# Kernel tuning notes

Measured on AMD Instinct MI355X. Metric: run time of the kernel, lower is better.

## Reference

```python
import jax, jax.numpy as jnp
import numpy as np
from jax import lax

STRIDE = 16
ANCHOR_BASE = 16
PRE_NMS = 6000
POST_NMS = 2000
NMS_THRESH = 0.7


def _generate_anchors(base_size=16, ratios=(0.5, 1.0, 2.0), scales=(8, 16, 32)):
    w = h = float(base_size)
    x_ctr = 0.5 * (w - 1)
    y_ctr = 0.5 * (h - 1)
    size = w * h
    anchors = []
    for r in ratios:
        ws = np.round(np.sqrt(size / r))
        hs = np.round(ws * r)
        for s in scales:
            wss, hss = ws * s, hs * s
            anchors.append([x_ctr - 0.5 * (wss - 1), y_ctr - 0.5 * (hss - 1),
                            x_ctr + 0.5 * (wss - 1), y_ctr + 0.5 * (hss - 1)])
    return np.array(anchors, dtype=np.float32)  # [9,4]


def _all_anchors(width, height, stride):
    base = _generate_anchors(ANCHOR_BASE)  # [A,4]
    sx = np.arange(width, dtype=np.float32) * stride
    gy, gx = np.meshgrid(np.arange(height, dtype=np.float32) * stride, sx, indexing='ij')
    shifts = np.stack([gx.ravel(), gy.ravel(), gx.ravel(), gy.ravel()], axis=1)  # [K,4] h-major
    return jnp.asarray((shifts[:, None, :] + base[None, :, :]).reshape(-1, 4))  # [K*A,4]


def setup_inputs() -> dict:
    key = jax.random.key(0)
    k1, k2 = jax.random.split(key)
    H = W = 64
    bbox_deltas = jax.random.normal(k1, (1, 36, H, W), dtype=jnp.float32)
    scores = jax.random.uniform(k2, (1, 2, 9 * H, W), dtype=jnp.float32)
    return {"bbox_deltas": bbox_deltas, "scores": scores, "im_w": 1024, "im_h": 1024}


def reference(bbox_deltas, scores, im_w, im_h):
    H, W = bbox_deltas.shape[2], bbox_deltas.shape[3]
    # fg scores: reshape [1,2,9H,W] -> [1,18,H,W], take channels 9:18
    sc = scores.reshape(1, 18, H, W)[:, 9:, :, :].transpose(0, 2, 3, 1).reshape(-1)
    dl = bbox_deltas.transpose(0, 2, 3, 1).reshape(-1, 4)
    anchors = _all_anchors(W, H, STRIDE)

    # bbox_transform_inv (decode)
    aw = anchors[:, 2] - anchors[:, 0] + 1.0
    ah = anchors[:, 3] - anchors[:, 1] + 1.0
    acx = anchors[:, 0] + 0.5 * aw
    acy = anchors[:, 1] + 0.5 * ah
    pcx = dl[:, 0] * aw + acx
    pcy = dl[:, 1] * ah + acy
    pw = jnp.exp(dl[:, 2]) * aw
    ph = jnp.exp(dl[:, 3]) * ah
    x1 = jnp.clip(pcx - 0.5 * pw, 0.0, im_w - 1.0)
    y1 = jnp.clip(pcy - 0.5 * ph, 0.0, im_h - 1.0)
    x2 = jnp.clip(pcx + 0.5 * pw, 0.0, im_w - 1.0)
    y2 = jnp.clip(pcy + 0.5 * ph, 0.0, im_h - 1.0)
    props = jnp.stack([x1, y1, x2, y2], axis=1)

    # min-size filter
    thresh = 16.0 * (float(im_h) / float(im_w))
    keep_f = ((x2 - x1 + 1.0) >= thresh) & ((y2 - y1 + 1.0) >= thresh)
    sc_m = jnp.where(keep_f, sc, -jnp.inf)

    # pre-NMS top-k by score
    top_sc, idx = lax.top_k(sc_m, PRE_NMS)
    top_p = props[idx]  # [PRE_NMS,4], sorted by score desc
    valid = jnp.isfinite(top_sc)

    # pairwise IoU (with +1 box convention, as in py_cpu_nms)
    bx1, by1, bx2, by2 = top_p[:, 0], top_p[:, 1], top_p[:, 2], top_p[:, 3]
    areas = (bx2 - bx1 + 1.0) * (by2 - by1 + 1.0)
    iw = jnp.maximum(jnp.minimum(bx2[:, None], bx2[None, :]) - jnp.maximum(bx1[:, None], bx1[None, :]) + 1.0, 0.0)
    ih = jnp.maximum(jnp.minimum(by2[:, None], by2[None, :]) - jnp.maximum(by1[:, None], by1[None, :]) + 1.0, 0.0)
    inter = iw * ih
    iou = inter / (areas[:, None] + areas[None, :] - inter)
    sup = iou > NMS_THRESH  # [N,N]

    ar = jnp.arange(PRE_NMS)

    def body(i, keep):
        row = sup[i] & keep[i] & (ar > i)
        return keep & (~row)

    keep = lax.fori_loop(0, PRE_NMS, body, valid)

    # take first POST_NMS kept (in score order), scatter into fixed-size output
    rank = jnp.cumsum(keep.astype(jnp.int32)) - 1
    sel = keep & (rank < POST_NMS)
    dst = jnp.where(sel, rank, POST_NMS)  # invalid rows dumped into slot POST_NMS
    out_b = jnp.zeros((POST_NMS + 1, 4), dtype=jnp.float32).at[dst].set(
        jnp.where(sel[:, None], top_p, 0.0))[:POST_NMS]
    out_s = jnp.zeros((POST_NMS + 1,), dtype=jnp.float32).at[dst].set(
        jnp.where(sel, top_sc, 0.0))[:POST_NMS]
    blob = jnp.concatenate([jnp.zeros((POST_NMS, 1), dtype=jnp.float32), out_b], axis=1)
    return blob, out_s[:, None]
```

## Files before the change

kernel.cpp:

```cpp
#include <hip/hip_runtime.h>
#include <math.h>

typedef unsigned int u32;
typedef unsigned long long u64;

#define NANCH   36864
#define PRE     6000
#define POST    2000
#define NWORDS  94

#define OFF_PROPS   ((size_t)0)
#define OFF_SV      ((size_t)589824)
#define OFF_TOPBOX  ((size_t)884736)
#define OFF_SORTED  ((size_t)980992)
#define OFF_SEL     ((size_t)1029120)
#define OFF_TOPKEY  ((size_t)1077248)
#define OFF_INVALW  ((size_t)1101312)
#define OFF_MASK    ((size_t)1102080)
#define OFF_ZERO    ((size_t)5614080)
#define OFF_H1      (OFF_ZERO)
#define OFF_H2      (OFF_H1 + 262144)
#define OFF_H3      (OFF_H2 + 262144)
#define OFF_CTRL    (OFF_H3 + 262144)
#define OFF_KEEPW   (OFF_CTRL + 256)
#define OFF_RANK    (OFF_KEEPW + 768)
#define ZERO_BYTES  ((size_t)(262144*3 + 256 + 768 + 24064))

__device__ __constant__ float BA[9][4] = {
  {-84.f,-40.f,99.f,55.f},   {-176.f,-88.f,191.f,103.f}, {-360.f,-184.f,375.f,199.f},
  {-56.f,-56.f,71.f,71.f},   {-120.f,-120.f,135.f,135.f},{-248.f,-248.f,263.f,263.f},
  {-36.f,-80.f,51.f,95.f},   {-80.f,-168.f,95.f,183.f},  {-168.f,-344.f,183.f,359.f}};

__global__ void decode_k(const float* __restrict__ deltas, const float* __restrict__ scores,
                         const int* __restrict__ imw_p, const int* __restrict__ imh_p,
                         float4* __restrict__ props, u64* __restrict__ sortvals) {
  #pragma clang fp contract(off)
  int i = blockIdx.x * 256 + threadIdx.x;
  if (i >= NANCH) return;
  int a = i % 9;
  int pix = i / 9;
  int x = pix & 63, y = pix >> 6;

  float sc = scores[(9 + a) * 4096 + pix];
  float d0 = deltas[(a * 4 + 0) * 4096 + pix];
  float d1 = deltas[(a * 4 + 1) * 4096 + pix];
  float d2 = deltas[(a * 4 + 2) * 4096 + pix];
  float d3 = deltas[(a * 4 + 3) * 4096 + pix];

  float gx = (float)(x * 16), gy = (float)(y * 16);
  float ax1 = gx + BA[a][0], ay1 = gy + BA[a][1];
  float ax2 = gx + BA[a][2], ay2 = gy + BA[a][3];
  float aw = ax2 - ax1 + 1.0f, ah = ay2 - ay1 + 1.0f;
  float acx = ax1 + 0.5f * aw, acy = ay1 + 0.5f * ah;

  float pcx = d0 * aw + acx;
  float pcy = d1 * ah + acy;
  float pw = (float)exp((double)d2) * aw;
  float ph = (float)exp((double)d3) * ah;

  float imw1 = (float)imw_p[0] - 1.0f, imh1 = (float)imh_p[0] - 1.0f;
  float x1 = fminf(fmaxf(pcx - 0.5f * pw, 0.0f), imw1);
  float y1 = fminf(fmaxf(pcy - 0.5f * ph, 0.0f), imh1);
  float x2 = fminf(fmaxf(pcx + 0.5f * pw, 0.0f), imw1);
  float y2 = fminf(fmaxf(pcy + 0.5f * ph, 0.0f), imh1);
  props[i] = make_float4(x1, y1, x2, y2);

  float thresh = 16.0f * ((float)imh_p[0] / (float)imw_p[0]);
  bool keep = (x2 - x1 + 1.0f >= thresh) && (y2 - y1 + 1.0f >= thresh);
  u32 key = keep ? (__float_as_uint(sc) | 0x80000000u) : 0u;
  sortvals[i] = ((u64)key << 32) | (u64)(0xFFFFFFFFu - (u32)i);
}

__global__ void hist_k(const u64* __restrict__ sv, u32* __restrict__ hist,
                       const u32* __restrict__ ctrl, int level) {
  int i = blockIdx.x * 256 + threadIdx.x;
  if (i >= NANCH) return;
  u64 v = sv[i];
  if (level == 1) {
    atomicAdd(&hist[(u32)(v >> 48)], 1u);
  } else if (level == 2) {
    if ((u32)(v >> 48) == ctrl[0]) atomicAdd(&hist[(u32)(v >> 32) & 0xFFFFu], 1u);
  } else {
    u32 pfx = (ctrl[0] << 16) | ctrl[2];
    if ((u32)(v >> 32) == pfx) atomicAdd(&hist[(u32)v & 0xFFFFu], 1u);
  }
}

__global__ void scan_k(const u32* __restrict__ hist, u32* __restrict__ ctrl, int level) {
  __shared__ u32 part[1024];
  int t = threadIdx.x;
  u32 ssum = 0;
  for (int b = 0; b < 64; ++b) ssum += hist[t * 64 + b];
  part[t] = ssum;
  __syncthreads();
  if (t == 0) {
    u32 Rin = (level == 1) ? (u32)PRE : ctrl[(level - 1) * 2 - 1];
    u32 acc = 0; int pt;
    for (pt = 1023; pt >= 0; --pt) {
      if (acc + part[pt] >= Rin) break;
      acc += part[pt];
    }
    int chosen = pt * 64; u32 Rout = Rin;
    for (int b = pt * 64 + 63; b >= pt * 64; --b) {
      u32 h = hist[b];
      if (acc + h >= Rin) { chosen = b; Rout = Rin - acc; break; }
      acc += h;
    }
    ctrl[(level - 1) * 2] = (u32)chosen;
    ctrl[(level - 1) * 2 + 1] = Rout;
    if (level == 3) {
      u64 T = ((u64)ctrl[0] << 48) | ((u64)ctrl[2] << 32) | 0xFFFF0000ULL | (u64)(u32)chosen;
      *(u64*)(&ctrl[8]) = T;
    }
  }
}

__global__ void compact_k(const u64* __restrict__ sv, u32* __restrict__ ctrl,
                          u64* __restrict__ sel) {
  int i = blockIdx.x * 256 + threadIdx.x;
  if (i >= NANCH) return;
  u64 T = *(const u64*)(&ctrl[8]);
  u64 v = sv[i];
  if (v >= T) {
    u32 p = atomicAdd(&ctrl[6], 1u);
    sel[p] = v;
  }
}

#define JCHUNK 1500
__global__ void rank_k(const u64* __restrict__ sel, u32* __restrict__ rank) {
  __shared__ u64 sj[256];
  int i = blockIdx.x * 256 + threadIdx.x;
  u64 vi = (i < PRE) ? sel[i] : 0ULL;
  int j0 = blockIdx.y * JCHUNK;
  int j1 = min(j0 + JCHUNK, PRE);
  u32 cnt = 0;
  for (int jb = j0; jb < j1; jb += 256) {
    int nj = min(256, j1 - jb);
    __syncthreads();
    if (threadIdx.x < nj) sj[threadIdx.x] = sel[jb + threadIdx.x];
    __syncthreads();
    #pragma unroll 8
    for (int j = 0; j < nj; ++j) cnt += (u32)(sj[j] > vi);
  }
  if (i < PRE && cnt) atomicAdd(&rank[i], cnt);
}

__global__ void rankscatter_k(const u64* __restrict__ sel, const u32* __restrict__ rank,
                              u64* __restrict__ sorted) {
  int i = blockIdx.x * 256 + threadIdx.x;
  if (i < PRE) sorted[rank[i]] = sel[i];
}

__global__ void gather_k(const u64* __restrict__ sorted, const float4* __restrict__ props,
                         float4* __restrict__ topbox, u32* __restrict__ topkey,
                         u64* __restrict__ invalw) {
  int r = blockIdx.x * 64 + threadIdx.x;
  u32 key = 0;
  if (r < PRE) {
    u64 v = sorted[r];
    key = (u32)(v >> 32);
    u32 idx = 0xFFFFu - ((u32)v & 0xFFFFu);
    topbox[r] = props[idx];
    topkey[r] = key;
  }
  u64 inval = __ballot(key == 0u);
  if (threadIdx.x == 0) invalw[blockIdx.x] = inval;
}

__global__ void mask_k(const float4* __restrict__ topbox, u64* __restrict__ mask) {
  #pragma clang fp contract(off)
  __shared__ float4 cb[64];
  int jb = blockIdx.x;
  if (jb < (int)blockIdx.y) return;
  int i = blockIdx.y * 64 + threadIdx.x;
  int jj = jb * 64 + threadIdx.x;
  cb[threadIdx.x] = (jj < PRE) ? topbox[jj] : make_float4(0.f, 0.f, 0.f, 0.f);
  __syncthreads();
  if (i >= PRE) return;
  float4 b = topbox[i];
  float ai = (b.z - b.x + 1.0f) * (b.w - b.y + 1.0f);
  u64 bits = 0ULL;
  int jmax = min(64, PRE - jb * 64);
  for (int j = 0; j < jmax; ++j) {
    float4 c = cb[j];
    float aj = (c.z - c.x + 1.0f) * (c.w - c.y + 1.0f);
    float iw = fmaxf(fminf(b.z, c.z) - fmaxf(b.x, c.x) + 1.0f, 0.0f);
    float ih = fmaxf(fminf(b.w, c.w) - fmaxf(b.y, c.y) + 1.0f, 0.0f);
    float inter = iw * ih;
    float iou = inter / (ai + aj - inter);
    bits |= ((u64)(iou > 0.7f)) << j;
  }
  mask[(size_t)i * NWORDS + jb] = bits;
}

__device__ __forceinline__ u64 rl64(u64 v, int lane) {
  u32 lo = (u32)__builtin_amdgcn_readlane((int)(u32)v, lane);
  u32 hi = (u32)__builtin_amdgcn_readlane((int)(u32)(v >> 32), lane);
  return ((u64)hi << 32) | (u64)lo;
}
__device__ __forceinline__ u64 rfl64(u64 v) {
  u32 lo = (u32)__builtin_amdgcn_readfirstlane((int)(u32)v);
  u32 hi = (u32)__builtin_amdgcn_readfirstlane((int)(u32)(v >> 32));
  return ((u64)hi << 32) | (u64)lo;
}

__global__ void __launch_bounds__(1024) nms_scan_k(const u64* __restrict__ mask,
                                                   const u64* __restrict__ invalw,
                                                   u64* __restrict__ keepw) {
  __shared__ u64 Lrem[NWORDS];
  __shared__ u64 Ldiag[64];
  __shared__ u64 Lkeep;
  __shared__ int Lstop;
  const int t = threadIdx.x;
  const int g = t >> 7;
  const int w = t & 127;
  const bool loader = (w < NWORDS);
  if (t < NWORDS) Lrem[t] = invalw[t];
  if (t == 0) Lstop = 0;
  u64 rv = 0;
  u64 B0[8], B1[8], B2[8];
  int kept = 0;

#define ISSUE(bb, BUF) \
  if ((bb) < NWORDS && loader) { \
    const int row0_ = (bb) * 64 + g * 8; \
    const u64* pp_ = mask + (size_t)row0_ * NWORDS + w; \
    _Pragma("unroll") \
    for (int j = 0; j < 8; ++j) { \
      bool ok_ = (w >= (bb)) && (row0_ + j < PRE); \
      BUF[j] = ok_ ? pp_[(size_t)j * NWORDS] : 0ULL; \
    } \
  }

#define STEP(bb, BUF, BUF2) { \
    if (w == (bb)) {                      \
      atomicOr((u32*)&Lrem[(bb)], (u32)rv); \
      atomicOr(((u32*)&Lrem[(bb)]) + 1, (u32)(rv >> 32)); \
      _Pragma("unroll") \
      for (int j = 0; j < 8; ++j) Ldiag[g * 8 + j] = BUF[j]; \
    } \
    __syncthreads();                      \
    ISSUE((bb) + 2, BUF2)                 \
    if (t < 64) { \
      u64 dgl = Ldiag[t]; \
      u64 avail = ~rfl64(Lrem[(bb)]);     \
      u64 kb = 0; \
      while (avail) { \
        int i_ = __builtin_ctzll(avail); \
        kb |= 1ULL << i_; \
        u64 di_ = rl64(dgl, i_); \
        avail &= ~di_ & ~((2ULL << i_) - 1ULL);  \
      } \
      if (t == 0) { \
        keepw[(bb)] = kb; \
        Lkeep = kb; \
        kept += (int)__popcll(kb); \
        if (kept >= POST) Lstop = 1; \
      } \
    } \
    __syncthreads();                      \
    { \
      u64 kb_ = Lkeep; \
      const int base_ = g * 8; \
      _Pragma("unroll") \
      for (int j = 0; j < 8; ++j) { \
        u64 k_ = (kb_ >> (base_ + j)) & 1ULL; \
        rv |= (0ULL - k_) & BUF[j]; \
      } \
    } \
    if (Lstop) break; }

  ISSUE(0, B0)
  ISSUE(1, B1)
  for (int bb = 0; bb < NWORDS; bb += 3) {
    STEP(bb, B0, B2)
    if (bb + 1 < NWORDS) STEP(bb + 1, B1, B0)
    if (bb + 2 < NWORDS) STEP(bb + 2, B2, B1)
  }
#undef ISSUE
#undef STEP
}

__global__ void scatter_k(const u64* __restrict__ keepw, const float4* __restrict__ topbox,
                          const u32* __restrict__ topkey, float* __restrict__ out) {
  __shared__ u64 wl[NWORDS];
  __shared__ u32 pre[NWORDS];
  int t = threadIdx.x;
  if (t < NWORDS) wl[t] = keepw[t];
  __syncthreads();
  if (t == 0) {
    u32 run = 0;
    for (int w = 0; w < NWORDS; ++w) { pre[w] = run; run += (u32)__popcll(wl[w]); }
  }
  __syncthreads();
  for (int i = t; i < PRE; i += 1024) {
    int w = i >> 6;
    u64 word = wl[w];
    if ((word >> (i & 63)) & 1ULL) {
      u32 rank = pre[w] + (u32)__popcll(word & ((1ULL << (i & 63)) - 1ULL));
      if (rank < POST) {
        float4 b = topbox[i];
        out[rank * 5 + 1] = b.x;
        out[rank * 5 + 2] = b.y;
        out[rank * 5 + 3] = b.z;
        out[rank * 5 + 4] = b.w;
        out[10000 + rank] = __uint_as_float(topkey[i] & 0x7FFFFFFFu);
      }
    }
  }
}

extern "C" void kernel_launch(void* const* d_in, const int* in_sizes, int n_in,
                              void* d_out, int out_size, void* d_ws, size_t ws_size,
                              hipStream_t stream) {
  const float* deltas = (const float*)d_in[0];
  const float* scores = (const float*)d_in[1];
  const int* imw = (const int*)d_in[2];
  const int* imh = (const int*)d_in[3];
  char* ws = (char*)d_ws;

  float4* props   = (float4*)(ws + OFF_PROPS);
  u64*    svals   = (u64*)(ws + OFF_SV);
  float4* topbox  = (float4*)(ws + OFF_TOPBOX);
  u64*    sorted  = (u64*)(ws + OFF_SORTED);
  u64*    sel     = (u64*)(ws + OFF_SEL);
  u32*    topkey  = (u32*)(ws + OFF_TOPKEY);
  u64*    invalw  = (u64*)(ws + OFF_INVALW);
  u64*    maskb   = (u64*)(ws + OFF_MASK);
  u32*    h1      = (u32*)(ws + OFF_H1);
  u32*    h2      = (u32*)(ws + OFF_H2);
  u32*    h3      = (u32*)(ws + OFF_H3);
  u32*    ctrl    = (u32*)(ws + OFF_CTRL);
  u64*    keepw   = (u64*)(ws + OFF_KEEPW);
  u32*    rankb   = (u32*)(ws + OFF_RANK);

  hipMemsetAsync(ws + OFF_ZERO, 0, ZERO_BYTES, stream);
  hipMemsetAsync(d_out, 0, 12000 * sizeof(float), stream);

  decode_k<<<144, 256, 0, stream>>>(deltas, scores, imw, imh, props, svals);

  hist_k<<<144, 256, 0, stream>>>(svals, h1, ctrl, 1);
  scan_k<<<1, 1024, 0, stream>>>(h1, ctrl, 1);
  hist_k<<<144, 256, 0, stream>>>(svals, h2, ctrl, 2);
  scan_k<<<1, 1024, 0, stream>>>(h2, ctrl, 2);
  hist_k<<<144, 256, 0, stream>>>(svals, h3, ctrl, 3);
  scan_k<<<1, 1024, 0, stream>>>(h3, ctrl, 3);

  compact_k<<<144, 256, 0, stream>>>(svals, ctrl, sel);

  dim3 rgrid(24, 4);
  rank_k<<<rgrid, 256, 0, stream>>>(sel, rankb);
  rankscatter_k<<<24, 256, 0, stream>>>(sel, rankb, sorted);

  gather_k<<<94, 64, 0, stream>>>(sorted, props, topbox, topkey, invalw);

  dim3 mgrid(NWORDS, NWORDS);
  mask_k<<<mgrid, 64, 0, stream>>>(topbox, maskb);

  nms_scan_k<<<1, 1024, 0, stream>>>(maskb, invalw, keepw);
  scatter_k<<<1, 1024, 0, stream>>>(keepw, topbox, topkey, (float*)d_out);
}
```

Measured before the change: 408.8 us.

## Fuse level-1 histogram into decode, parallelize radix scan, deepen NMS prefetch

The level-1 histogram atomic moves into the decode kernel, which removes one launch and one pass over the sort values. The threshold-finding scan replaces its serial single-thread search with wavefront shuffle reductions and a ballot. The NMS scan kernel swaps __syncthreads for a raw s_waitcnt lgkmcnt(0) plus s_barrier, and prefetches mask rows three steps ahead with four buffers instead of three. The custom barrier does not wait on global memory counters, which is safe only because the barrier-protected shared state lives in LDS. The extra buffer raises register pressure.

After: 456.3 us. +11.6%, slower.

```diff
diff --git a/kernel.cpp b/kernel.cpp
--- a/kernel.cpp
+++ b/kernel.cpp
@@ -33,7 +33,8 @@
 
 __global__ void decode_k(const float* __restrict__ deltas, const float* __restrict__ scores,
                          const int* __restrict__ imw_p, const int* __restrict__ imh_p,
-                         float4* __restrict__ props, u64* __restrict__ sortvals) {
+                         float4* __restrict__ props, u64* __restrict__ sortvals,
+                         u32* __restrict__ h1) {
   #pragma clang fp contract(off)
   int i = blockIdx.x * 256 + threadIdx.x;
   if (i >= NANCH) return;
@@ -69,6 +70,7 @@
   bool keep = (x2 - x1 + 1.0f >= thresh) && (y2 - y1 + 1.0f >= thresh);
   u32 key = keep ? (__float_as_uint(sc) | 0x80000000u) : 0u;
   sortvals[i] = ((u64)key << 32) | (u64)(0xFFFFFFFFu - (u32)i);
+  atomicAdd(&h1[key >> 16], 1u);
 }
 
 __global__ void hist_k(const u64* __restrict__ sv, u32* __restrict__ hist,
@@ -76,9 +78,7 @@
   int i = blockIdx.x * 256 + threadIdx.x;
   if (i >= NANCH) return;
   u64 v = sv[i];
-  if (level == 1) {
-    atomicAdd(&hist[(u32)(v >> 48)], 1u);
-  } else if (level == 2) {
+  if (level == 2) {
     if ((u32)(v >> 48) == ctrl[0]) atomicAdd(&hist[(u32)(v >> 32) & 0xFFFFu], 1u);
   } else {
     u32 pfx = (ctrl[0] << 16) | ctrl[2];
@@ -86,31 +86,65 @@
   }
 }
 
-__global__ void scan_k(const u32* __restrict__ hist, u32* __restrict__ ctrl, int level) {
+__global__ void __launch_bounds__(1024) scan_k(const u32* __restrict__ hist,
+                                               u32* __restrict__ ctrl, int level) {
   __shared__ u32 part[1024];
-  int t = threadIdx.x;
-  u32 ssum = 0;
-  for (int b = 0; b < 64; ++b) ssum += hist[t * 64 + b];
-  part[t] = ssum;
-  __syncthreads();
-  if (t == 0) {
-    u32 Rin = (level == 1) ? (u32)PRE : ctrl[(level - 1) * 2 - 1];
-    u32 acc = 0; int pt;
-    for (pt = 1023; pt >= 0; --pt) {
-      if (acc + part[pt] >= Rin) break;
-      acc += part[pt];
+  __shared__ u32 wtot[16], wsfx[16];
+  __shared__ int cgrp;
+  __shared__ u32 ghi;
+  const int t = threadIdx.x, w = t >> 6, l = t & 63;
+
+  for (int k = 0; k < 64; ++k) {
+    int gg = w + (k << 4);
+    u32 v = hist[gg * 64 + l];
+    for (int off = 32; off; off >>= 1) v += __shfl_down(v, off);
+    if (l == 0) part[gg] = v;
+  }
+  __syncthreads();
+
+  u32 v = part[t];
+  for (int off = 1; off < 64; off <<= 1) {
+    u32 o = __shfl_down(v, off);
+    if (l + off < 64) v += o;
+  }
+  if (l == 0) wtot[w] = v;
+  __syncthreads();
+  if (w == 0 && l < 16) {
+    u32 x = wtot[l];
+    for (int off = 1; off < 16; off <<= 1) {
+      u32 o = __shfl_down(x, off);
+      if (l + off < 16) x += o;
     }
-    int chosen = pt * 64; u32 Rout = Rin;
-    for (int b = pt * 64 + 63; b >= pt * 64; --b) {
-      u32 h = hist[b];
-      if (acc + h >= Rin) { chosen = b; Rout = Rin - acc; break; }
-      acc += h;
+    wsfx[l] = x;
+  }
+  __syncthreads();
+
+  u32 Rin = (level == 1) ? (u32)PRE : ctrl[(level - 1) * 2 - 1];
+  u32 G = v + ((w < 15) ? wsfx[w + 1] : 0);
+  u32 p = part[t];
+  if (G >= Rin && G - p < Rin) { cgrp = t; ghi = G - p; }
+  __syncthreads();
+
+  if (w == 0) {
+    int gg = cgrp;
+    u32 h = hist[gg * 64 + l];
+    u32 s = h;
+    for (int off = 1; off < 64; off <<= 1) {
+      u32 o = __shfl_down(s, off);
+      if (l + off < 64) s += o;
     }
-    ctrl[(level - 1) * 2] = (u32)chosen;
-    ctrl[(level - 1) * 2 + 1] = Rout;
-    if (level == 3) {
-      u64 T = ((u64)ctrl[0] << 48) | ((u64)ctrl[2] << 32) | 0xFFFF0000ULL | (u64)(u32)chosen;
-      *(u64*)(&ctrl[8]) = T;
+    u32 S = s + ghi;
+    u64 m = __ballot(S >= Rin);
+    int cb = 63 - __builtin_clzll(m);
+    if (l == cb) {
+      u32 Rout = Rin - (S - h);
+      int chosen = gg * 64 + cb;
+      ctrl[(level - 1) * 2] = (u32)chosen;
+      ctrl[(level - 1) * 2 + 1] = Rout;
+      if (level == 3) {
+        u64 T = ((u64)ctrl[0] << 48) | ((u64)ctrl[2] << 32) | 0xFFFF0000ULL | (u64)(u32)chosen;
+        *(u64*)(&ctrl[8]) = T;
+      }
     }
   }
 }
@@ -194,6 +228,9 @@
   mask[(size_t)i * NWORDS + jb] = bits;
 }
 
+__device__ __forceinline__ void wg_barrier() {
+  __asm__ volatile("s_waitcnt lgkmcnt(0)\n\ts_barrier" ::: "memory");
+}
 __device__ __forceinline__ u64 rl64(u64 v, int lane) {
   u32 lo = (u32)__builtin_amdgcn_readlane((int)(u32)v, lane);
   u32 hi = (u32)__builtin_amdgcn_readlane((int)(u32)(v >> 32), lane);
@@ -219,7 +256,7 @@
   if (t < NWORDS) Lrem[t] = invalw[t];
   if (t == 0) Lstop = 0;
   u64 rv = 0;
-  u64 B0[8], B1[8], B2[8];
+  u64 B0[8], B1[8], B2[8], B3[8];
   int kept = 0;
 
 #define ISSUE(bb, BUF) \
@@ -233,15 +270,15 @@
     } \
   }
 
-#define STEP(bb, BUF, BUF2) { \
+#define STEP(bb, BUF, BUFN) { \
     if (w == (bb)) {                      \
       atomicOr((u32*)&Lrem[(bb)], (u32)rv); \
       atomicOr(((u32*)&Lrem[(bb)]) + 1, (u32)(rv >> 32)); \
       _Pragma("unroll") \
       for (int j = 0; j < 8; ++j) Ldiag[g * 8 + j] = BUF[j]; \
     } \
-    __syncthreads();                      \
-    ISSUE((bb) + 2, BUF2)                 \
+    wg_barrier();                         \
+    ISSUE((bb) + 3, BUFN)                 \
     if (t < 64) { \
       u64 dgl = Ldiag[t]; \
       u64 avail = ~rfl64(Lrem[(bb)]);     \
@@ -259,7 +296,7 @@
         if (kept >= POST) Lstop = 1; \
       } \
     } \
-    __syncthreads();                      \
+    wg_barrier();                         \
     { \
       u64 kb_ = Lkeep; \
       const int base_ = g * 8; \
@@ -273,10 +310,12 @@
 
   ISSUE(0, B0)
   ISSUE(1, B1)
-  for (int bb = 0; bb < NWORDS; bb += 3) {
-    STEP(bb, B0, B2)
+  ISSUE(2, B2)
+  for (int bb = 0; bb < NWORDS; bb += 4) {
+    STEP(bb, B0, B3)
     if (bb + 1 < NWORDS) STEP(bb + 1, B1, B0)
     if (bb + 2 < NWORDS) STEP(bb + 2, B2, B1)
+    if (bb + 3 < NWORDS) STEP(bb + 3, B3, B2)
   }
 #undef ISSUE
 #undef STEP
@@ -338,9 +377,7 @@
   hipMemsetAsync(ws + OFF_ZERO, 0, ZERO_BYTES, stream);
   hipMemsetAsync(d_out, 0, 12000 * sizeof(float), stream);
 
-  decode_k<<<144, 256, 0, stream>>>(deltas, scores, imw, imh, props, svals);
-
-  hist_k<<<144, 256, 0, stream>>>(svals, h1, ctrl, 1);
+  decode_k<<<144, 256, 0, stream>>>(deltas, scores, imw, imh, props, svals, h1);
   scan_k<<<1, 1024, 0, stream>>>(h1, ctrl, 1);
   hist_k<<<144, 256, 0, stream>>>(svals, h2, ctrl, 2);
   scan_k<<<1, 1024, 0, stream>>>(h2, ctrl, 2);
```

## Collapse radix top-k into fused coarse histogram, single-pass rank sort, and fewer launches

Applied to the files above, without the earlier changes.

Replaces the three-level histogram/scan radix select with one coarse 1024-bin histogram built inside the decode kernel and a single-wavefront scan that picks a cutoff bin. A superset of candidates is compacted and ranked in one all-pairs pass that writes the sorted array and the invalid bitmap directly. The separate rank-scatter, gather, and output memset steps are dropped, with mask and output kernels indexing props through the sorted keys. The NMS scan now prefetches three blocks ahead and skips loading rows already suppressed. Together these cut the kernel launch count and the dependent serial phases, at the cost of ranking a larger candidate set and doing indirect gathers in the mask kernel.

New measurement: 334.6 us. -18.2%, faster.

```diff
diff --git a/kernel.cpp b/kernel.cpp
--- a/kernel.cpp
+++ b/kernel.cpp
@@ -11,29 +11,30 @@
 
 #define OFF_PROPS   ((size_t)0)
 #define OFF_SV      ((size_t)589824)
-#define OFF_TOPBOX  ((size_t)884736)
-#define OFF_SORTED  ((size_t)980992)
-#define OFF_SEL     ((size_t)1029120)
-#define OFF_TOPKEY  ((size_t)1077248)
-#define OFF_INVALW  ((size_t)1101312)
-#define OFF_MASK    ((size_t)1102080)
-#define OFF_ZERO    ((size_t)5614080)
-#define OFF_H1      (OFF_ZERO)
-#define OFF_H2      (OFF_H1 + 262144)
-#define OFF_H3      (OFF_H2 + 262144)
-#define OFF_CTRL    (OFF_H3 + 262144)
-#define OFF_KEEPW   (OFF_CTRL + 256)
-#define OFF_RANK    (OFF_KEEPW + 768)
-#define ZERO_BYTES  ((size_t)(262144*3 + 256 + 768 + 24064))
+#define OFF_SORTED  ((size_t)884736)
+#define OFF_SEL     ((size_t)932864)
+#define OFF_MASK    ((size_t)1227776)
+#define OFF_CTRL    ((size_t)5739776)
+#define OFF_H1      ((size_t)5740032)
+#define OFF_INVALW  ((size_t)5744384)
+#define OFF_KEEPW   ((size_t)5745152)
+#define ZERO_BYTES  ((size_t)(256 + 4352 + 768))
 
 __device__ __constant__ float BA[9][4] = {
   {-84.f,-40.f,99.f,55.f},   {-176.f,-88.f,191.f,103.f}, {-360.f,-184.f,375.f,199.f},
   {-56.f,-56.f,71.f,71.f},   {-120.f,-120.f,135.f,135.f},{-248.f,-248.f,263.f,263.f},
   {-36.f,-80.f,51.f,95.f},   {-80.f,-168.f,95.f,183.f},  {-168.f,-344.f,183.f,359.f}};
 
+__device__ __forceinline__ u32 key_bin(u32 key) {
+  if (key < 0xBF000000u) return 0u;
+  u32 b = ((key >> 13) - 0x5F800u) + 1u;
+  return b > 1024u ? 1024u : b;
+}
+
 __global__ void decode_k(const float* __restrict__ deltas, const float* __restrict__ scores,
                          const int* __restrict__ imw_p, const int* __restrict__ imh_p,
-                         float4* __restrict__ props, u64* __restrict__ sortvals) {
+                         float4* __restrict__ props, u64* __restrict__ sortvals,
+                         u32* __restrict__ h1) {
   #pragma clang fp contract(off)
   int i = blockIdx.x * 256 + threadIdx.x;
   if (i >= NANCH) return;
@@ -69,49 +70,32 @@
   bool keep = (x2 - x1 + 1.0f >= thresh) && (y2 - y1 + 1.0f >= thresh);
   u32 key = keep ? (__float_as_uint(sc) | 0x80000000u) : 0u;
   sortvals[i] = ((u64)key << 32) | (u64)(0xFFFFFFFFu - (u32)i);
-}
-
-__global__ void hist_k(const u64* __restrict__ sv, u32* __restrict__ hist,
-                       const u32* __restrict__ ctrl, int level) {
-  int i = blockIdx.x * 256 + threadIdx.x;
-  if (i >= NANCH) return;
-  u64 v = sv[i];
-  if (level == 1) {
-    atomicAdd(&hist[(u32)(v >> 48)], 1u);
-  } else if (level == 2) {
-    if ((u32)(v >> 48) == ctrl[0]) atomicAdd(&hist[(u32)(v >> 32) & 0xFFFFu], 1u);
-  } else {
-    u32 pfx = (ctrl[0] << 16) | ctrl[2];
-    if ((u32)(v >> 32) == pfx) atomicAdd(&hist[(u32)v & 0xFFFFu], 1u);
-  }
-}
-
-__global__ void scan_k(const u32* __restrict__ hist, u32* __restrict__ ctrl, int level) {
-  __shared__ u32 part[1024];
-  int t = threadIdx.x;
-  u32 ssum = 0;
-  for (int b = 0; b < 64; ++b) ssum += hist[t * 64 + b];
-  part[t] = ssum;
-  __syncthreads();
-  if (t == 0) {
-    u32 Rin = (level == 1) ? (u32)PRE : ctrl[(level - 1) * 2 - 1];
-    u32 acc = 0; int pt;
-    for (pt = 1023; pt >= 0; --pt) {
-      if (acc + part[pt] >= Rin) break;
-      acc += part[pt];
-    }
-    int chosen = pt * 64; u32 Rout = Rin;
-    for (int b = pt * 64 + 63; b >= pt * 64; --b) {
-      u32 h = hist[b];
-      if (acc + h >= Rin) { chosen = b; Rout = Rin - acc; break; }
-      acc += h;
-    }
-    ctrl[(level - 1) * 2] = (u32)chosen;
-    ctrl[(level - 1) * 2 + 1] = Rout;
-    if (level == 3) {
-      u64 T = ((u64)ctrl[0] << 48) | ((u64)ctrl[2] << 32) | 0xFFFF0000ULL | (u64)(u32)chosen;
-      *(u64*)(&ctrl[8]) = T;
-    }
+  u32 bin = key_bin(key);
+  if (bin) atomicAdd(&h1[bin], 1u);
+}
+
+__global__ void scan_k(const u32* __restrict__ h1, u32* __restrict__ ctrl) {
+  int l = threadIdx.x;
+  u32 loc[16], suf[16];
+  #pragma unroll
+  for (int k = 0; k < 16; ++k) loc[k] = h1[1 + l * 16 + k];
+  u32 acc = 0;
+  #pragma unroll
+  for (int k = 15; k >= 0; --k) { acc += loc[k]; suf[k] = acc; }
+  u32 sfx = acc;
+  for (int off = 1; off < 64; off <<= 1) {
+    u32 o = __shfl_down(sfx, off);
+    if (l + off < 64) sfx += o;
+  }
+  u32 S_above = sfx - acc;
+  u64 mball = __ballot(suf[0] + S_above >= (u32)PRE);
+  if (mball == 0ULL) { if (l == 0) ctrl[0] = 0u; return; }
+  int L = 63 - __builtin_clzll(mball);
+  if (l == L) {
+    int kk = 0;
+    for (int k = 15; k >= 0; --k)
+      if (suf[k] + S_above >= (u32)PRE) { kk = k; break; }
+    ctrl[0] = (u32)(1 + 16 * L + kk);
   }
 }
 
@@ -119,66 +103,55 @@
                           u64* __restrict__ sel) {
   int i = blockIdx.x * 256 + threadIdx.x;
   if (i >= NANCH) return;
-  u64 T = *(const u64*)(&ctrl[8]);
+  u32 chosen = ctrl[0];
   u64 v = sv[i];
-  if (v >= T) {
+  if (key_bin((u32)(v >> 32)) >= chosen) {
     u32 p = atomicAdd(&ctrl[6], 1u);
     sel[p] = v;
   }
 }
 
-#define JCHUNK 1500
-__global__ void rank_k(const u64* __restrict__ sel, u32* __restrict__ rank) {
+__global__ void rank_k(const u64* __restrict__ sel, const u32* __restrict__ ctrl,
+                       u64* __restrict__ sorted, u64* __restrict__ invalw) {
   __shared__ u64 sj[256];
+  u32 n = ctrl[6];
   int i = blockIdx.x * 256 + threadIdx.x;
-  u64 vi = (i < PRE) ? sel[i] : 0ULL;
-  int j0 = blockIdx.y * JCHUNK;
-  int j1 = min(j0 + JCHUNK, PRE);
+  if ((u32)(blockIdx.x * 256) >= n) return;
+  u64 vi = ((u32)i < n) ? sel[i] : 0ULL;
   u32 cnt = 0;
-  for (int jb = j0; jb < j1; jb += 256) {
-    int nj = min(256, j1 - jb);
+  for (u32 jb = 0; jb < n; jb += 256) {
     __syncthreads();
-    if (threadIdx.x < nj) sj[threadIdx.x] = sel[jb + threadIdx.x];
+    if (jb + threadIdx.x < n) sj[threadIdx.x] = sel[jb + threadIdx.x];
     __syncthreads();
+    u32 m = min(256u, n - jb);
     #pragma unroll 8
-    for (int j = 0; j < nj; ++j) cnt += (u32)(sj[j] > vi);
-  }
-  if (i < PRE && cnt) atomicAdd(&rank[i], cnt);
-}
-
-__global__ void rankscatter_k(const u64* __restrict__ sel, const u32* __restrict__ rank,
-                              u64* __restrict__ sorted) {
-  int i = blockIdx.x * 256 + threadIdx.x;
-  if (i < PRE) sorted[rank[i]] = sel[i];
-}
-
-__global__ void gather_k(const u64* __restrict__ sorted, const float4* __restrict__ props,
-                         float4* __restrict__ topbox, u32* __restrict__ topkey,
-                         u64* __restrict__ invalw) {
-  int r = blockIdx.x * 64 + threadIdx.x;
-  u32 key = 0;
-  if (r < PRE) {
-    u64 v = sorted[r];
-    key = (u32)(v >> 32);
-    u32 idx = 0xFFFFu - ((u32)v & 0xFFFFu);
-    topbox[r] = props[idx];
-    topkey[r] = key;
-  }
-  u64 inval = __ballot(key == 0u);
-  if (threadIdx.x == 0) invalw[blockIdx.x] = inval;
-}
-
-__global__ void mask_k(const float4* __restrict__ topbox, u64* __restrict__ mask) {
+    for (u32 j = 0; j < m; ++j) cnt += (u32)(sj[j] > vi);
+  }
+  if ((u32)i < n && cnt < (u32)PRE) {
+    sorted[cnt] = vi;
+    if ((u32)(vi >> 32) == 0u)
+      atomicOr((unsigned long long*)&invalw[cnt >> 6], 1ULL << (cnt & 63));
+  }
+}
+
+__global__ void mask_k(const u64* __restrict__ sorted, const float4* __restrict__ props,
+                       u64* __restrict__ mask) {
   #pragma clang fp contract(off)
   __shared__ float4 cb[64];
   int jb = blockIdx.x;
   if (jb < (int)blockIdx.y) return;
   int i = blockIdx.y * 64 + threadIdx.x;
   int jj = jb * 64 + threadIdx.x;
-  cb[threadIdx.x] = (jj < PRE) ? topbox[jj] : make_float4(0.f, 0.f, 0.f, 0.f);
+  float4 cc = make_float4(0.f, 0.f, 0.f, 0.f);
+  if (jj < PRE) {
+    u64 v = sorted[jj];
+    cc = props[0xFFFFu - ((u32)v & 0xFFFFu)];
+  }
+  cb[threadIdx.x] = cc;
   __syncthreads();
   if (i >= PRE) return;
-  float4 b = topbox[i];
+  u64 vi = sorted[i];
+  float4 b = props[0xFFFFu - ((u32)vi & 0xFFFFu)];
   float ai = (b.z - b.x + 1.0f) * (b.w - b.y + 1.0f);
   u64 bits = 0ULL;
   int jmax = min(64, PRE - jb * 64);
@@ -212,36 +185,42 @@
   __shared__ u64 Ldiag[64];
   __shared__ u64 Lkeep;
   __shared__ int Lstop;
+  __shared__ int Llast;
   const int t = threadIdx.x;
   const int g = t >> 7;
   const int w = t & 127;
   const bool loader = (w < NWORDS);
   if (t < NWORDS) Lrem[t] = invalw[t];
-  if (t == 0) Lstop = 0;
+  if (t == 0) { Lstop = 0; Llast = NWORDS - 1; }
   u64 rv = 0;
   u64 B0[8], B1[8], B2[8];
   int kept = 0;
+  __syncthreads();
 
 #define ISSUE(bb, BUF) \
   if ((bb) < NWORDS && loader) { \
+    u64 st_ = Lrem[(bb)]; \
     const int row0_ = (bb) * 64 + g * 8; \
     const u64* pp_ = mask + (size_t)row0_ * NWORDS + w; \
     _Pragma("unroll") \
     for (int j = 0; j < 8; ++j) { \
-      bool ok_ = (w >= (bb)) && (row0_ + j < PRE); \
+      bool ok_ = (w >= (bb)) && (row0_ + j < PRE) && !((st_ >> (g * 8 + j)) & 1ULL); \
       BUF[j] = ok_ ? pp_[(size_t)j * NWORDS] : 0ULL; \
     } \
   }
 
-#define STEP(bb, BUF, BUF2) { \
+#define STEP(bb, BUF) { \
     if (w == (bb)) {                      \
       atomicOr((u32*)&Lrem[(bb)], (u32)rv); \
       atomicOr(((u32*)&Lrem[(bb)]) + 1, (u32)(rv >> 32)); \
       _Pragma("unroll") \
       for (int j = 0; j < 8; ++j) Ldiag[g * 8 + j] = BUF[j]; \
     } \
+    if ((bb) + 3 < NWORDS && w == (bb) + 3) {   \
+      atomicOr((u32*)&Lrem[(bb) + 3], (u32)rv); \
+      atomicOr(((u32*)&Lrem[(bb) + 3]) + 1, (u32)(rv >> 32)); \
+    } \
     __syncthreads();                      \
-    ISSUE((bb) + 2, BUF2)                 \
     if (t < 64) { \
       u64 dgl = Ldiag[t]; \
       u64 avail = ~rfl64(Lrem[(bb)]);     \
@@ -256,7 +235,7 @@
         keepw[(bb)] = kb; \
         Lkeep = kb; \
         kept += (int)__popcll(kb); \
-        if (kept >= POST) Lstop = 1; \
+        if (kept >= POST) { Lstop = 1; Llast = (bb); } \
       } \
     } \
     __syncthreads();                      \
@@ -269,24 +248,32 @@
         rv |= (0ULL - k_) & BUF[j]; \
       } \
     } \
+    ISSUE((bb) + 3, BUF)                  \
     if (Lstop) break; }
 
   ISSUE(0, B0)
   ISSUE(1, B1)
+  ISSUE(2, B2)
   for (int bb = 0; bb < NWORDS; bb += 3) {
-    STEP(bb, B0, B2)
-    if (bb + 1 < NWORDS) STEP(bb + 1, B1, B0)
-    if (bb + 2 < NWORDS) STEP(bb + 2, B2, B1)
+    STEP(bb, B0)
+    if (bb + 1 < NWORDS) STEP(bb + 1, B1)
+    if (bb + 2 < NWORDS) STEP(bb + 2, B2)
   }
 #undef ISSUE
 #undef STEP
-}
-
-__global__ void scatter_k(const u64* __restrict__ keepw, const float4* __restrict__ topbox,
-                          const u32* __restrict__ topkey, float* __restrict__ out) {
+
+  __syncthreads();
+  int last = Llast;
+  for (int w2 = t; w2 < NWORDS; w2 += 1024)
+    if (w2 > last) keepw[w2] = 0ULL;
+}
+
+__global__ void outscatter_k(const u64* __restrict__ keepw, const u64* __restrict__ sorted,
+                             const float4* __restrict__ props, float* __restrict__ out) {
   __shared__ u64 wl[NWORDS];
   __shared__ u32 pre[NWORDS];
   int t = threadIdx.x;
+  for (int i = t; i < 12000; i += 1024) out[i] = 0.0f;
   if (t < NWORDS) wl[t] = keepw[t];
   __syncthreads();
   if (t == 0) {
@@ -300,12 +287,13 @@
     if ((word >> (i & 63)) & 1ULL) {
       u32 rank = pre[w] + (u32)__popcll(word & ((1ULL << (i & 63)) - 1ULL));
       if (rank < POST) {
-        float4 b = topbox[i];
+        u64 v = sorted[i];
+        float4 b = props[0xFFFFu - ((u32)v & 0xFFFFu)];
         out[rank * 5 + 1] = b.x;
         out[rank * 5 + 2] = b.y;
         out[rank * 5 + 3] = b.z;
         out[rank * 5 + 4] = b.w;
-        out[10000 + rank] = __uint_as_float(topkey[i] & 0x7FFFFFFFu);
+        out[10000 + rank] = __uint_as_float((u32)(v >> 32) & 0x7FFFFFFFu);
       }
     }
   }
@@ -322,42 +310,24 @@
 
   float4* props   = (float4*)(ws + OFF_PROPS);
   u64*    svals   = (u64*)(ws + OFF_SV);
-  float4* topbox  = (float4*)(ws + OFF_TOPBOX);
   u64*    sorted  = (u64*)(ws + OFF_SORTED);
   u64*    sel     = (u64*)(ws + OFF_SEL);
-  u32*    topkey  = (u32*)(ws + OFF_TOPKEY);
+  u64*    maskb   = (u64*)(ws + OFF_MASK);
+  u32*    ctrl    = (u32*)(ws + OFF_CTRL);
+  u32*    h1      = (u32*)(ws + OFF_H1);
   u64*    invalw  = (u64*)(ws + OFF_INVALW);
-  u64*    maskb   = (u64*)(ws + OFF_MASK);
-  u32*    h1      = (u32*)(ws + OFF_H1);
-  u32*    h2      = (u32*)(ws + OFF_H2);
-  u32*    h3      = (u32*)(ws + OFF_H3);
-  u32*    ctrl    = (u32*)(ws + OFF_CTRL);
   u64*    keepw   = (u64*)(ws + OFF_KEEPW);
-  u32*    rankb   = (u32*)(ws + OFF_RANK);
-
-  hipMemsetAsync(ws + OFF_ZERO, 0, ZERO_BYTES, stream);
-  hipMemsetAsync(d_out, 0, 12000 * sizeof(float), stream);
-
-  decode_k<<<144, 256, 0, stream>>>(deltas, scores, imw, imh, props, svals);
-
-  hist_k<<<144, 256, 0, stream>>>(svals, h1, ctrl, 1);
-  scan_k<<<1, 1024, 0, stream>>>(h1, ctrl, 1);
-  hist_k<<<144, 256, 0, stream>>>(svals, h2, ctrl, 2);
-  scan_k<<<1, 1024, 0, stream>>>(h2, ctrl, 2);
-  hist_k<<<144, 256, 0, stream>>>(svals, h3, ctrl, 3);
-  scan_k<<<1, 1024, 0, stream>>>(h3, ctrl, 3);
-
+
+  hipMemsetAsync(ws + OFF_CTRL, 0, ZERO_BYTES, stream);
+
+  decode_k<<<144, 256, 0, stream>>>(deltas, scores, imw, imh, props, svals, h1);
+  scan_k<<<1, 64, 0, stream>>>(h1, ctrl);
   compact_k<<<144, 256, 0, stream>>>(svals, ctrl, sel);
-
-  dim3 rgrid(24, 4);
-  rank_k<<<rgrid, 256, 0, stream>>>(sel, rankb);
-  rankscatter_k<<<24, 256, 0, stream>>>(sel, rankb, sorted);
-
-  gather_k<<<94, 64, 0, stream>>>(sorted, props, topbox, topkey, invalw);
+  rank_k<<<144, 256, 0, stream>>>(sel, ctrl, sorted, invalw);
 
   dim3 mgrid(NWORDS, NWORDS);
-  mask_k<<<mgrid, 64, 0, stream>>>(topbox, maskb);
+  mask_k<<<mgrid, 64, 0, stream>>>(sorted, props, maskb);
 
   nms_scan_k<<<1, 1024, 0, stream>>>(maskb, invalw, keepw);
-  scatter_k<<<1, 1024, 0, stream>>>(keepw, topbox, topkey, (float*)d_out);
-}
+  outscatter_k<<<1, 1024, 0, stream>>>(keepw, sorted, props, (float*)d_out);
+}
```
